# Kernel tuning notes

Hardware: AMD Instinct MI355X
Metric: run time of the kernel (lower is better)

## Reference

```python
import jax, jax.numpy as jnp
import numpy as np

B, J, D, H = 4096, 17, 512, 8
DK = D // H  # 64
NEG = jnp.float32(-9e15)


def _build_adj_mask():
    # Human3.6M 17-joint skeleton (parent indices), symmetric + self-loops,
    # matching SemGCN's adj>0 mask (adj_mx_from_edges adds identity).
    parents = np.array([-1, 0, 1, 2, 0, 4, 5, 0, 7, 8, 9, 8, 11, 12, 8, 14, 15])
    A = np.eye(J, dtype=np.float32)
    for c, p in enumerate(parents):
        if p >= 0:
            A[c, p] = 1.0
            A[p, c] = 1.0
    rows, cols = np.nonzero(A)
    return rows.astype(np.int32), cols.astype(np.int32)


def setup_inputs() -> dict:
    key = jax.random.key(0)
    ks = jax.random.split(key, 16)
    s = 0.02
    rows, cols = _build_adj_mask()
    return {
        "src": jax.random.normal(ks[0], (B, J, D), jnp.float32),
        # per-head Q/K/V Linears, stacked over heads: [H, D, DK]
        "Wq": jax.random.normal(ks[1], (H, D, DK), jnp.float32) * s,
        "bq": jnp.zeros((H, DK), jnp.float32),
        "Wk": jax.random.normal(ks[2], (H, D, DK), jnp.float32) * s,
        "bk": jnp.zeros((H, DK), jnp.float32),
        "Wv": jax.random.normal(ks[3], (H, D, DK), jnp.float32) * s,
        "bv": jnp.zeros((H, DK), jnp.float32),
        # output projection of MultiHeadAttention: [H*DK, D]
        "Wo": jax.random.normal(ks[4], (H * DK, D), jnp.float32) * s,
        "bo": jnp.zeros((D,), jnp.float32),
        "ln1_g": jnp.ones((D,), jnp.float32),
        "ln1_b": jnp.zeros((D,), jnp.float32),
        # SemGraphConv: two weight matrices [2, D, D], edge logits e, bias
        "W_gcn": jax.random.normal(ks[5], (2, D, D), jnp.float32) * s,
        "e_gcn": jax.random.normal(ks[6], (rows.shape[0],), jnp.float32),
        "b_gcn": jnp.zeros((D,), jnp.float32),
        "ln2_g": jnp.ones((D,), jnp.float32),
        "ln2_b": jnp.zeros((D,), jnp.float32),
        "mask_rows": jnp.asarray(rows),
        "mask_cols": jnp.asarray(cols),
    }


def _layernorm(x, g, b, eps=1e-5):
    mu = jnp.mean(x, axis=-1, keepdims=True)
    var = jnp.var(x, axis=-1, keepdims=True)
    return (x - mu) * jax.lax.rsqrt(var + eps) * g + b


def _forward(src, Wq, bq, Wk, bk, Wv, bv, Wo, bo, ln1_g, ln1_b,
             W_gcn, e_gcn, b_gcn, ln2_g, ln2_b, mask_rows, mask_cols):
    # --- multi-head attention (all heads vectorized) ---
    q = jnp.einsum('bjd,hde->bhje', src, Wq) + bq[None, :, None, :]
    k = jnp.einsum('bjd,hde->bhje', src, Wk) + bk[None, :, None, :]
    v = jnp.einsum('bjd,hde->bhje', src, Wv) + bv[None, :, None, :]
    scale = jnp.float32(DK) ** 0.5  # q.size(-1) ** 0.5
    att = jax.nn.softmax(jnp.einsum('bhje,bhke->bhjk', q, k) / scale, axis=-1)
    o = jnp.einsum('bhjk,bhke->bhje', att, v)          # [B,H,J,DK]
    o = o.transpose(0, 2, 1, 3).reshape(B, J, H * DK)  # concat over heads
    attn_out = o @ Wo + bo
    x = _layernorm(src + attn_out, ln1_g, ln1_b)

    # --- SemGraphConv ---
    h0 = x @ W_gcn[0]
    h1 = x @ W_gcn[1]
    logits = jnp.full((J, J), NEG, jnp.float32).at[mask_rows, mask_cols].set(e_gcn)
    A = jax.nn.softmax(logits, axis=1)                 # [J,J]
    I = jnp.eye(J, dtype=jnp.float32)
    gcn = jnp.einsum('jk,bkd->bjd', A * I, h0) + jnp.einsum('jk,bkd->bjd', A * (1.0 - I), h1)
    gcn = gcn + b_gcn
    return _layernorm(x + gcn, ln2_g, ln2_b)


def reference(src, Wq, bq, Wk, bk, Wv, bv, Wo, bo, ln1_g, ln1_b,
              W_gcn, e_gcn, b_gcn, ln2_g, ln2_b, mask_rows, mask_cols):
    return _forward(src, Wq, bq, Wk, bk, Wv, bv, Wo, bo, ln1_g, ln1_b,
                    W_gcn, e_gcn, b_gcn, ln2_g, ln2_b, mask_rows, mask_cols)
```

## Files before the change

### kernel.cpp

```cpp
#include <hip/hip_runtime.h>


typedef __attribute__((ext_vector_type(4))) float floatx4;
typedef __attribute__((ext_vector_type(8))) short short8;

#define AS1 __attribute__((address_space(1)))
#define AS3 __attribute__((address_space(3)))

__device__ __forceinline__ float bf2f(unsigned short u) {
  union { unsigned int i; float f; } x;
  x.i = ((unsigned int)u) << 16;
  return x.f;
}

__device__ __forceinline__ unsigned short f2bf(float f) {
  union { float f; unsigned int i; } x;
  x.f = f;
  unsigned int r = x.i + 0x7fffu + ((x.i >> 16) & 1u);
  return (unsigned short)(r >> 16);
}

__device__ __forceinline__ void unpack8(uint4 u, float* f) {
  unsigned int uu[4] = {u.x, u.y, u.z, u.w};
#pragma unroll
  for (int i = 0; i < 4; ++i) {
    f[2 * i]     = bf2f((unsigned short)(uu[i] & 0xffffu));
    f[2 * i + 1] = bf2f((unsigned short)(uu[i] >> 16));
  }
}

__device__ __forceinline__ uint4 pack8(const float* f) {
  unsigned int uu[4];
#pragma unroll
  for (int i = 0; i < 4; ++i)
    uu[i] = (unsigned int)f2bf(f[2 * i]) | ((unsigned int)f2bf(f[2 * i + 1]) << 16);
  uint4 u; u.x = uu[0]; u.y = uu[1]; u.z = uu[2]; u.w = uu[3];
  return u;
}

__device__ __forceinline__ float wave_sum(float v) {
#pragma unroll
  for (int m = 1; m < 64; m <<= 1) v += __shfl_xor(v, m, 64);
  return v;
}

__device__ __forceinline__ void gload_lds16(const unsigned short* g, AS3 char* l) {
  __builtin_amdgcn_global_load_lds((const AS1 void*)g, (AS3 void*)l, 16, 0, 0);
}

__global__ __launch_bounds__(256) void convert_src(
    const float* __restrict__ in, unsigned short* __restrict__ out) {
  const size_t i = ((size_t)blockIdx.x * 256 + threadIdx.x) * 8;
  const float4 a = *(const float4*)(in + i);
  const float4 b = *(const float4*)(in + i + 4);
  const float f[8] = {a.x, a.y, a.z, a.w, b.x, b.y, b.z, b.w};
  *(uint4*)(out + i) = pack8(f);
}

__global__ __launch_bounds__(256) void gemm_bt(
    const unsigned short* __restrict__ A,
    const unsigned short* __restrict__ BT,
    const float* __restrict__ bias,
    unsigned short* __restrict__ C, int N) {
  __shared__ unsigned short As[128 * 32];
  __shared__ unsigned short Bs[128 * 32];
  const int t = threadIdx.x;
  const int wave = t >> 6;
  const int lane = t & 63;
  const int wm = wave >> 1, wn = wave & 1;
  const long rowBase = (long)blockIdx.x * 128;
  const long colBase = (long)blockIdx.y * 128;

  const unsigned short* a0 = A + (size_t)rowBase * 512;
  const unsigned short* b0 = BT + (size_t)colBase * 512;

  floatx4 acc[4][4];
#pragma unroll
  for (int i = 0; i < 4; ++i)
#pragma unroll
    for (int j = 0; j < 4; ++j) acc[i][j] = (floatx4){0.f, 0.f, 0.f, 0.f};

  const size_t gOff0 = ((size_t)(t >> 2)) * 512 + (size_t)(t & 3) * 8;
  const size_t gOff1 = ((size_t)((t + 256) >> 2)) * 512 + (size_t)(t & 3) * 8;
  AS3 char* AsL = (AS3 char*)As;
  AS3 char* BsL = (AS3 char*)Bs;
  const int ldsOff0 = wave * 1024;
  const int ldsOff1 = 4096 + wave * 1024;

  const int am = lane & 15;
  const int aq = (lane >> 4) << 3;

  for (int k0 = 0; k0 < 512; k0 += 32) {
    __syncthreads();
    gload_lds16(a0 + gOff0 + k0, AsL + ldsOff0);
    gload_lds16(a0 + gOff1 + k0, AsL + ldsOff1);
    gload_lds16(b0 + gOff0 + k0, BsL + ldsOff0);
    gload_lds16(b0 + gOff1 + k0, BsL + ldsOff1);
    __syncthreads();

    short8 af[4], bf[4];
#pragma unroll
    for (int i = 0; i < 4; ++i)
      af[i] = *(const short8*)&As[(wm * 64 + i * 16 + am) * 32 + aq];
#pragma unroll
    for (int j = 0; j < 4; ++j)
      bf[j] = *(const short8*)&Bs[(wn * 64 + j * 16 + am) * 32 + aq];
#pragma unroll
    for (int i = 0; i < 4; ++i)
#pragma unroll
      for (int j = 0; j < 4; ++j)
        acc[i][j] = __builtin_amdgcn_mfma_f32_16x16x32_bf16(af[i], bf[j], acc[i][j], 0, 0, 0);
  }

  const int q4 = (lane >> 4) << 2;
#pragma unroll
  for (int i = 0; i < 4; ++i) {
#pragma unroll
    for (int j = 0; j < 4; ++j) {
      const long col = colBase + wn * 64 + j * 16 + am;
      const float badd = bias ? bias[col] : 0.f;
      const long rowa = rowBase + wm * 64 + i * 16 + q4;
#pragma unroll
      for (int r = 0; r < 4; ++r)
        C[(size_t)(rowa + r) * N + col] = f2bf(acc[i][j][r] + badd);
    }
  }
}

__global__ __launch_bounds__(256) void attn_kernel(
    const unsigned short* __restrict__ qkv, unsigned short* __restrict__ o) {
  const int b = blockIdx.x, h = blockIdx.y;
  __shared__ float q[17][65], k[17][65], v[17][65];
  __shared__ float S[17][17];
  const int t = threadIdx.x;
  const unsigned short* base = qkv + (size_t)b * 17 * 1536 + h * 64;

  for (int idx = t; idx < 3 * 136; idx += 256) {
    const int m = idx / 136, rem = idx - m * 136;
    const int r = rem >> 3, e0 = (rem & 7) << 3;
    uint4 u = *(const uint4*)(base + (size_t)r * 1536 + m * 512 + e0);
    float f[8];
    unpack8(u, f);
    float(*dst)[65] = (m == 0) ? q : (m == 1) ? k : v;
#pragma unroll
    for (int e = 0; e < 8; ++e) dst[r][e0 + e] = f[e];
  }
  __syncthreads();

  for (int idx = t; idx < 289; idx += 256) {
    const int j = idx / 17, kk = idx - j * 17;
    float s = 0.f;
#pragma unroll 8
    for (int e = 0; e < 64; ++e) s += q[j][e] * k[kk][e];
    S[j][kk] = s * 0.125f;
  }
  __syncthreads();

  if (t < 17) {
    float m = -1e30f;
#pragma unroll
    for (int kk = 0; kk < 17; ++kk) m = fmaxf(m, S[t][kk]);
    float tmp[17], sum = 0.f;
#pragma unroll
    for (int kk = 0; kk < 17; ++kk) { tmp[kk] = __expf(S[t][kk] - m); sum += tmp[kk]; }
    const float inv = 1.f / sum;
#pragma unroll
    for (int kk = 0; kk < 17; ++kk) S[t][kk] = tmp[kk] * inv;
  }
  __syncthreads();

  unsigned short* ob = o + (size_t)b * 17 * 512 + h * 64;
  for (int idx = t; idx < 136; idx += 256) {
    const int j = idx >> 3, e0 = (idx & 7) << 3;
    float ov[8] = {0, 0, 0, 0, 0, 0, 0, 0};
#pragma unroll
    for (int kk = 0; kk < 17; ++kk) {
      const float a = S[j][kk];
#pragma unroll
      for (int e = 0; e < 8; ++e) ov[e] += a * v[kk][e0 + e];
    }
    *(uint4*)(ob + (size_t)j * 512 + e0) = pack8(ov);
  }
}

__global__ __launch_bounds__(256) void ln_res_kernel(
    const float* __restrict__ a, const unsigned short* __restrict__ b,
    const float* __restrict__ g, const float* __restrict__ beta,
    unsigned short* __restrict__ out) {
  const long row = (long)blockIdx.x * 4 + (threadIdx.x >> 6);
  const int lane = threadIdx.x & 63;
  const int d0 = lane * 8;

  const float4 a0 = *(const float4*)(a + (size_t)row * 512 + d0);
  const float4 a1 = *(const float4*)(a + (size_t)row * 512 + d0 + 4);
  const float fa[8] = {a0.x, a0.y, a0.z, a0.w, a1.x, a1.y, a1.z, a1.w};
  float fb[8], vals[8];
  unpack8(*(const uint4*)(b + (size_t)row * 512 + d0), fb);
  float s = 0.f, s2 = 0.f;
#pragma unroll
  for (int i = 0; i < 8; ++i) {
    vals[i] = fa[i] + fb[i];
    s += vals[i];
    s2 += vals[i] * vals[i];
  }
  const float mean = wave_sum(s) * (1.f / 512.f);
  const float var = wave_sum(s2) * (1.f / 512.f) - mean * mean;
  const float rs = rsqrtf(var + 1e-5f);

  const float4 g0 = *(const float4*)(g + d0);
  const float4 g1 = *(const float4*)(g + d0 + 4);
  const float4 b0 = *(const float4*)(beta + d0);
  const float4 b1 = *(const float4*)(beta + d0 + 4);
  const float fg[8]  = {g0.x, g0.y, g0.z, g0.w, g1.x, g1.y, g1.z, g1.w};
  const float fbt[8] = {b0.x, b0.y, b0.z, b0.w, b1.x, b1.y, b1.z, b1.w};
  float y[8];
#pragma unroll
  for (int i = 0; i < 8; ++i) y[i] = (vals[i] - mean) * rs * fg[i] + fbt[i];
  *(uint4*)(out + (size_t)row * 512 + d0) = pack8(y);
}

__global__ __launch_bounds__(256) void gcn_ln_kernel(
    const unsigned short* __restrict__ x, const unsigned short* __restrict__ h01,
    const float* __restrict__ Adiag, const int* __restrict__ cnt,
    const int* __restrict__ nbrk, const float* __restrict__ nbrw,
    const float* __restrict__ bgcn,
    const float* __restrict__ g, const float* __restrict__ beta,
    float* __restrict__ out) {
  const long row = (long)blockIdx.x * 4 + (threadIdx.x >> 6);
  const int lane = threadIdx.x & 63;
  const int b = (int)(row / 17);
  const int j = (int)(row - (long)b * 17);
  const int d0 = lane * 8;

  float accv[8];
  {
    const float w = Adiag[j];
    float f[8];
    unpack8(*(const uint4*)(h01 + (size_t)row * 1024 + d0), f);
#pragma unroll
    for (int i = 0; i < 8; ++i) accv[i] = w * f[i];
  }
  const int c = cnt[j];
  for (int nb = 0; nb < c; ++nb) {
    const int kk = nbrk[j * 8 + nb];
    const float w = nbrw[j * 8 + nb];
    float f[8];
    unpack8(*(const uint4*)(h01 + ((size_t)b * 17 + kk) * 1024 + 512 + d0), f);
#pragma unroll
    for (int i = 0; i < 8; ++i) accv[i] += w * f[i];
  }

  float fx[8], vals[8];
  unpack8(*(const uint4*)(x + (size_t)row * 512 + d0), fx);
  const float4 bg0 = *(const float4*)(bgcn + d0);
  const float4 bg1 = *(const float4*)(bgcn + d0 + 4);
  const float fbg[8] = {bg0.x, bg0.y, bg0.z, bg0.w, bg1.x, bg1.y, bg1.z, bg1.w};
  float s = 0.f, s2 = 0.f;
#pragma unroll
  for (int i = 0; i < 8; ++i) {
    vals[i] = fx[i] + accv[i] + fbg[i];
    s += vals[i];
    s2 += vals[i] * vals[i];
  }
  const float mean = wave_sum(s) * (1.f / 512.f);
  const float var = wave_sum(s2) * (1.f / 512.f) - mean * mean;
  const float rs = rsqrtf(var + 1e-5f);

  const float4 g0 = *(const float4*)(g + d0);
  const float4 g1 = *(const float4*)(g + d0 + 4);
  const float4 bb0 = *(const float4*)(beta + d0);
  const float4 bb1 = *(const float4*)(beta + d0 + 4);
  const float fg[8]  = {g0.x, g0.y, g0.z, g0.w, g1.x, g1.y, g1.z, g1.w};
  const float fbt[8] = {bb0.x, bb0.y, bb0.z, bb0.w, bb1.x, bb1.y, bb1.z, bb1.w};
  float4 y0, y1;
  y0.x = (vals[0] - mean) * rs * fg[0] + fbt[0];
  y0.y = (vals[1] - mean) * rs * fg[1] + fbt[1];
  y0.z = (vals[2] - mean) * rs * fg[2] + fbt[2];
  y0.w = (vals[3] - mean) * rs * fg[3] + fbt[3];
  y1.x = (vals[4] - mean) * rs * fg[4] + fbt[4];
  y1.y = (vals[5] - mean) * rs * fg[5] + fbt[5];
  y1.z = (vals[6] - mean) * rs * fg[6] + fbt[6];
  y1.w = (vals[7] - mean) * rs * fg[7] + fbt[7];
  *(float4*)(out + (size_t)row * 512 + d0) = y0;
  *(float4*)(out + (size_t)row * 512 + d0 + 4) = y1;
}

__global__ __launch_bounds__(256) void prep_transpose(
    const float* __restrict__ Wq, const float* __restrict__ Wk,
    const float* __restrict__ Wv, const float* __restrict__ Wo,
    const float* __restrict__ Wg,
    unsigned short* __restrict__ WT1, unsigned short* __restrict__ WT2,
    unsigned short* __restrict__ WT3) {
  const int idx = blockIdx.x * 256 + threadIdx.x;
  if (idx < 786432) {
    const int n = idx >> 9, k = idx & 511;
    const int which = n >> 9, nn = n & 511;
    const int hh = nn >> 6, e = nn & 63;
    const float* W = (which == 0) ? Wq : (which == 1) ? Wk : Wv;
    WT1[idx] = f2bf(W[hh * 32768 + k * 64 + e]);
  } else if (idx < 786432 + 262144) {
    const int i2 = idx - 786432;
    const int n = i2 >> 9, k = i2 & 511;
    WT2[i2] = f2bf(Wo[k * 512 + n]);
  } else {
    const int i3 = idx - 1048576;
    const int n = i3 >> 9, k = i3 & 511;
    const int which = n >> 9, nn = n & 511;
    WT3[i3] = f2bf(Wg[which * 262144 + k * 512 + nn]);
  }
}

__global__ __launch_bounds__(256) void prep_small(
    const float* __restrict__ bq, const float* __restrict__ bk,
    const float* __restrict__ bv, const float* __restrict__ bo,
    const float* __restrict__ e, const int* __restrict__ rows,
    const int* __restrict__ cols, int nnz,
    float* __restrict__ bias1, float* __restrict__ bias2,
    float* __restrict__ Adiag, int* __restrict__ cnt,
    int* __restrict__ nbrk, float* __restrict__ nbrw) {
  const int t = threadIdx.x;
  for (int i = t; i < 1536; i += 256)
    bias1[i] = (i < 512) ? bq[i] : (i < 1024) ? bk[i - 512] : bv[i - 1024];
  for (int i = t; i < 512; i += 256) bias2[i] = bo[i];
  if (t < 17) {
    float m = -1e30f;
    for (int i = 0; i < nnz; ++i)
      if (rows[i] == t) m = fmaxf(m, e[i]);
    float s = 0.f;
    for (int i = 0; i < nnz; ++i)
      if (rows[i] == t) s += __expf(e[i] - m);
    const float inv = 1.f / s;
    int c = 0;
    for (int i = 0; i < nnz; ++i)
      if (rows[i] == t) {
        const float w = __expf(e[i] - m) * inv;
        const int kk = cols[i];
        if (kk == t) Adiag[t] = w;
        else { nbrk[t * 8 + c] = kk; nbrw[t * 8 + c] = w; ++c; }
      }
    cnt[t] = c;
  }
}

extern "C" void kernel_launch(void* const* d_in, const int* in_sizes, int n_in,
                              void* d_out, int out_size, void* d_ws, size_t ws_size,
                              hipStream_t stream) {
  const float* src = (const float*)d_in[0];
  const float* Wq  = (const float*)d_in[1];
  const float* bq  = (const float*)d_in[2];
  const float* Wk  = (const float*)d_in[3];
  const float* bk  = (const float*)d_in[4];
  const float* Wv  = (const float*)d_in[5];
  const float* bv  = (const float*)d_in[6];
  const float* Wo  = (const float*)d_in[7];
  const float* bo  = (const float*)d_in[8];
  const float* ln1g = (const float*)d_in[9];
  const float* ln1b = (const float*)d_in[10];
  const float* Wg  = (const float*)d_in[11];
  const float* eg  = (const float*)d_in[12];
  const float* bg  = (const float*)d_in[13];
  const float* ln2g = (const float*)d_in[14];
  const float* ln2b = (const float*)d_in[15];
  const int* mrows = (const int*)d_in[16];
  const int* mcols = (const int*)d_in[17];
  const int nnz = in_sizes[16];

  float* out = (float*)d_out;
  char* ws = (char*)d_ws;

  unsigned short* WT1 = (unsigned short*)(ws + 0x0000000);
  unsigned short* WT2 = (unsigned short*)(ws + 0x0180000);
  unsigned short* WT3 = (unsigned short*)(ws + 0x0200000);
  float* bias1 = (float*)(ws + 0x0300000);
  float* bias2 = (float*)(ws + 0x0302000);
  float* Adiag = (float*)(ws + 0x0303000);
  int* cnt     = (int*)(ws + 0x0303100);
  int* nbrk    = (int*)(ws + 0x0303200);
  float* nbrw  = (float*)(ws + 0x0303600);
  unsigned short* SRCB = (unsigned short*)(ws + 0x0400000);
  unsigned short* QKV  = (unsigned short*)(ws + 0x4800000);
  unsigned short* O    = (unsigned short*)(ws + 0x0400000);
  unsigned short* ATT  = (unsigned short*)(ws + 0x4800000);
  unsigned short* X    = (unsigned short*)(ws + 0x8C00000);
  unsigned short* H01  = (unsigned short*)(ws + 0x0400000);

  (void)n_in; (void)out_size; (void)ws_size;

  convert_src<<<17408, 256, 0, stream>>>(src, SRCB);
  prep_transpose<<<6144, 256, 0, stream>>>(Wq, Wk, Wv, Wo, Wg, WT1, WT2, WT3);
  prep_small<<<1, 256, 0, stream>>>(bq, bk, bv, bo, eg, mrows, mcols, nnz,
                                    bias1, bias2, Adiag, cnt, nbrk, nbrw);
  gemm_bt<<<dim3(544, 12), 256, 0, stream>>>(SRCB, WT1, bias1, QKV, 1536);
  attn_kernel<<<dim3(4096, 8), 256, 0, stream>>>(QKV, O);
  gemm_bt<<<dim3(544, 4), 256, 0, stream>>>(O, WT2, bias2, ATT, 512);
  ln_res_kernel<<<17408, 256, 0, stream>>>(src, ATT, ln1g, ln1b, X);
  gemm_bt<<<dim3(544, 8), 256, 0, stream>>>(X, WT3, nullptr, H01, 1024);
  gcn_ln_kernel<<<17408, 256, 0, stream>>>(X, H01, Adiag, cnt, nbrk, nbrw, bg,
                                           ln2g, ln2b, out);
}
```

Baseline: 937.6 us.

## Triple-buffer GEMM LDS loads, swizzle LDS layout, remap blocks for XCD locality

The bf16 GEMM now uses a three-stage LDS ring, issuing direct global-to-LDS loads two k-tiles ahead and waiting with explicit vmcnt counts so memory latency overlaps the MFMA work. The 16-byte chunks inside each LDS row are XOR-swizzled to reduce bank conflicts on fragment reads. A 1D grid is remapped so consecutive tiles land on the same XCD, which should improve L2 reuse. In exchange LDS use triples, and the hand-written waitcnt logic relies on the compiler not reordering the loads.

```diff
diff --git a/kernel.cpp b/kernel.cpp
--- a/kernel.cpp
+++ b/kernel.cpp
@@ -62,14 +62,20 @@
     const unsigned short* __restrict__ BT,
     const float* __restrict__ bias,
     unsigned short* __restrict__ C, int N) {
-  __shared__ unsigned short As[128 * 32];
-  __shared__ unsigned short Bs[128 * 32];
+  __shared__ unsigned short As[3][128 * 32];
+  __shared__ unsigned short Bs[3][128 * 32];
   const int t = threadIdx.x;
   const int wave = t >> 6;
   const int lane = t & 63;
   const int wm = wave >> 1, wn = wave & 1;
-  const long rowBase = (long)blockIdx.x * 128;
-  const long colBase = (long)blockIdx.y * 128;
+
+  const int nTN = N >> 7;
+  const int q8 = gridDim.x >> 3;
+  const int lin = (blockIdx.x & 7) * q8 + (blockIdx.x >> 3);
+  const int tm = lin / nTN;
+  const int tn = lin - tm * nTN;
+  const long rowBase = (long)tm * 128;
+  const long colBase = (long)tn * 128;
 
   const unsigned short* a0 = A + (size_t)rowBase * 512;
   const unsigned short* b0 = BT + (size_t)colBase * 512;
@@ -80,37 +86,61 @@
 #pragma unroll
     for (int j = 0; j < 4; ++j) acc[i][j] = (floatx4){0.f, 0.f, 0.f, 0.f};
 
-  const size_t gOff0 = ((size_t)(t >> 2)) * 512 + (size_t)(t & 3) * 8;
-  const size_t gOff1 = ((size_t)((t + 256) >> 2)) * 512 + (size_t)(t & 3) * 8;
-  AS3 char* AsL = (AS3 char*)As;
-  AS3 char* BsL = (AS3 char*)Bs;
-  const int ldsOff0 = wave * 1024;
-  const int ldsOff1 = 4096 + wave * 1024;
+  const int c0 = t, c1 = t + 256;
+  const size_t gOff0 =
+      (size_t)(c0 >> 2) * 512 + (size_t)((c0 & 3) ^ ((c0 >> 3) & 3)) * 8;
+  const size_t gOff1 =
+      (size_t)(c1 >> 2) * 512 + (size_t)((c1 & 3) ^ ((c1 >> 3) & 3)) * 8;
+  const int ldsByte0 = wave * 1024;
+  const int ldsByte1 = 4096 + wave * 1024;
+
+#define STAGE(buf, k0)                                                       \
+  do {                                                                       \
+    gload_lds16(a0 + gOff0 + (k0), (AS3 char*)&As[(buf)][0] + ldsByte0);     \
+    gload_lds16(a0 + gOff1 + (k0), (AS3 char*)&As[(buf)][0] + ldsByte1);     \
+    gload_lds16(b0 + gOff0 + (k0), (AS3 char*)&Bs[(buf)][0] + ldsByte0);     \
+    gload_lds16(b0 + gOff1 + (k0), (AS3 char*)&Bs[(buf)][0] + ldsByte1);     \
+  } while (0)
 
   const int am = lane & 15;
-  const int aq = (lane >> 4) << 3;
-
-  for (int k0 = 0; k0 < 512; k0 += 32) {
-    __syncthreads();
-    gload_lds16(a0 + gOff0 + k0, AsL + ldsOff0);
-    gload_lds16(a0 + gOff1 + k0, AsL + ldsOff1);
-    gload_lds16(b0 + gOff0 + k0, BsL + ldsOff0);
-    gload_lds16(b0 + gOff1 + k0, BsL + ldsOff1);
-    __syncthreads();
-
+  const int q = lane >> 4;
+
+  STAGE(0, 0);
+  STAGE(1, 32);
+  asm volatile("s_waitcnt vmcnt(4)" ::: "memory");
+  __builtin_amdgcn_sched_barrier(0);
+  __builtin_amdgcn_s_barrier();
+
+#pragma unroll
+  for (int kt = 0; kt < 16; ++kt) {
+    if (kt + 2 < 16) STAGE((kt + 2) % 3, (kt + 2) * 32);
+
+    const unsigned short* As_ = &As[kt % 3][0];
+    const unsigned short* Bs_ = &Bs[kt % 3][0];
     short8 af[4], bf[4];
 #pragma unroll
-    for (int i = 0; i < 4; ++i)
-      af[i] = *(const short8*)&As[(wm * 64 + i * 16 + am) * 32 + aq];
-#pragma unroll
-    for (int j = 0; j < 4; ++j)
-      bf[j] = *(const short8*)&Bs[(wn * 64 + j * 16 + am) * 32 + aq];
+    for (int i = 0; i < 4; ++i) {
+      const int row = wm * 64 + i * 16 + am;
+      af[i] = *(const short8*)&As_[row * 32 + ((q ^ ((row >> 1) & 3)) << 3)];
+    }
+#pragma unroll
+    for (int j = 0; j < 4; ++j) {
+      const int row = wn * 64 + j * 16 + am;
+      bf[j] = *(const short8*)&Bs_[row * 32 + ((q ^ ((row >> 1) & 3)) << 3)];
+    }
 #pragma unroll
     for (int i = 0; i < 4; ++i)
 #pragma unroll
       for (int j = 0; j < 4; ++j)
         acc[i][j] = __builtin_amdgcn_mfma_f32_16x16x32_bf16(af[i], bf[j], acc[i][j], 0, 0, 0);
-  }
+
+    if (kt == 15) break;
+    if (kt < 14) asm volatile("s_waitcnt vmcnt(4)" ::: "memory");
+    else         asm volatile("s_waitcnt vmcnt(0)" ::: "memory");
+    __builtin_amdgcn_sched_barrier(0);
+    __builtin_amdgcn_s_barrier();
+  }
+#undef STAGE
 
   const int q4 = (lane >> 4) << 2;
 #pragma unroll
@@ -390,11 +420,11 @@
   prep_transpose<<<6144, 256, 0, stream>>>(Wq, Wk, Wv, Wo, Wg, WT1, WT2, WT3);
   prep_small<<<1, 256, 0, stream>>>(bq, bk, bv, bo, eg, mrows, mcols, nnz,
                                     bias1, bias2, Adiag, cnt, nbrk, nbrw);
-  gemm_bt<<<dim3(544, 12), 256, 0, stream>>>(SRCB, WT1, bias1, QKV, 1536);
+  gemm_bt<<<6528, 256, 0, stream>>>(SRCB, WT1, bias1, QKV, 1536);
   attn_kernel<<<dim3(4096, 8), 256, 0, stream>>>(QKV, O);
-  gemm_bt<<<dim3(544, 4), 256, 0, stream>>>(O, WT2, bias2, ATT, 512);
+  gemm_bt<<<2176, 256, 0, stream>>>(O, WT2, bias2, ATT, 512);
   ln_res_kernel<<<17408, 256, 0, stream>>>(src, ATT, ln1g, ln1b, X);
-  gemm_bt<<<dim3(544, 8), 256, 0, stream>>>(X, WT3, nullptr, H01, 1024);
+  gemm_bt<<<4352, 256, 0, stream>>>(X, WT3, nullptr, H01, 1024);
   gcn_ln_kernel<<<17408, 256, 0, stream>>>(X, H01, Adiag, cnt, nbrk, nbrw, bg,
                                            ln2g, ln2b, out);
 }
```

After: 906.4 us. 1.03x faster.
